# Optimization experiments

Measured on AMD Instinct MI355X. Metric: run time of the kernel, lower is better.

## Reference

```python
import jax, jax.numpy as jnp
import numpy as np

DIM = 256
N_CHANNELS = 8
NEIGHBORS = 16


def setup_inputs() -> dict:
    key = jax.random.key(0)
    kx, kw = jax.random.split(key)
    B, N, D = 4, 1024, DIM
    x = jax.random.normal(kx, (B, N, D), dtype=jnp.float32)
    # nn.Linear(dim, dim*2*n_channels, bias=False); store as [in, out] so y = x @ W
    W_qk = jax.random.normal(kw, (D, 2 * N_CHANNELS * D), dtype=jnp.float32) * (D ** -0.5)
    return {"x": x, "W_qk": W_qk}


def _norm_edge(edge):
    # edge: [B, C, N, N]
    norm_row = edge / (edge.sum(axis=-1, keepdims=True) + 1e-6)
    norm_col = norm_row / (norm_row.sum(axis=-2, keepdims=True) + 1e-6)
    # norm_row @ norm_col^T
    return jnp.einsum('bcnk,bcmk->bcnm', norm_row, norm_col)


def reference(x, W_qk):
    B, N, D = x.shape
    C = N_CHANNELS
    scale = D ** -0.5
    qk = (x @ W_qk).reshape(B, N, 2, C, D)
    q = jnp.transpose(qk[:, :, 0], (0, 2, 1, 3))  # [B, C, N, D]
    k = jnp.transpose(qk[:, :, 1], (0, 2, 1, 3))  # [B, C, N, D]
    attn = jax.nn.softmax(jnp.einsum('bcnd,bcmd->bcnm', q, k) * scale, axis=-1)

    # clip(): top-k neighbor mask from channel-summed (detached) attention
    sum_edge = jax.lax.stop_gradient(attn).sum(axis=1)  # [B, N, N]
    kk = min(NEIGHBORS, N)
    _, top_idx = jax.lax.top_k(sum_edge, kk)  # [B, N, kk]
    b_idx = jnp.arange(B)[:, None, None]
    r_idx = jnp.arange(N)[None, :, None]
    mask = jnp.zeros((B, N, N), dtype=attn.dtype).at[b_idx, r_idx, top_idx].set(1.0)
    mask = jnp.maximum(mask, jnp.eye(N, dtype=attn.dtype))  # identity diag
    edge = mask[:, None] * attn  # [B, C, N, N]
    return _norm_edge(edge)
```

## Files before the change

kernel.cpp:

```cpp
#include <hip/hip_runtime.h>
#include <hip/hip_bf16.h>
#include <math.h>

#define BB 4
#define NN 1024
#define DD 256
#define CC 8
#define KNBR 16
#define MAXSEL 17
#define ZCAP (NN * MAXSEL)

typedef _Float16 f16x8_t __attribute__((ext_vector_type(8)));
typedef _Float16 f16x4_t __attribute__((ext_vector_type(4)));
typedef float    f32x4_t __attribute__((ext_vector_type(4)));

__device__ __forceinline__ void gl2lds16(const _Float16* g, _Float16* ldsbase) {
    __builtin_amdgcn_global_load_lds(
        (const __attribute__((address_space(1))) unsigned int*)g,
        (__attribute__((address_space(3))) unsigned int*)ldsbase, 16, 0, 0);
}

__device__ __forceinline__ void split2(float v, _Float16& h, _Float16& l) {
    h = (_Float16)v;
    l = (_Float16)(v - (float)h);
}

__global__ __launch_bounds__(256) void split_all(const float* __restrict__ x,
                                                 const float* __restrict__ W,
                                                 _Float16* __restrict__ xh,
                                                 _Float16* __restrict__ xl,
                                                 _Float16* __restrict__ Wth,
                                                 _Float16* __restrict__ Wtl,
                                                 int* __restrict__ countb) {
    const int tid = threadIdx.x;
    if (blockIdx.x < 1024) {
        int i = (blockIdx.x * 256 + tid) * 4;
        float4 v = *(const float4*)(x + i);
        f16x4_t hv, lv;
        _Float16 h, l;
        split2(v.x, h, l); hv[0] = h; lv[0] = l;
        split2(v.y, h, l); hv[1] = h; lv[1] = l;
        split2(v.z, h, l); hv[2] = h; lv[2] = l;
        split2(v.w, h, l); hv[3] = h; lv[3] = l;
        *(f16x4_t*)(xh + i) = hv;
        *(f16x4_t*)(xl + i) = lv;
    } else {
        const int b2 = blockIdx.x - 1024;
        if (b2 == 0) {
            int4 zz = make_int4(0, 0, 0, 0);
#pragma unroll
            for (int g = 0; g < 4; g++) ((int4*)countb)[tid + 256 * g] = zz;
        }
        __shared__ float t[64][65];
        const int n0 = (b2 & 63) * 64;
        const int k0 = (b2 >> 6) * 64;
#pragma unroll
        for (int i = 0; i < 16; i++) {
            int k = i * 4 + (tid >> 6);
            int n = tid & 63;
            t[k][n] = W[(size_t)(k0 + k) * 4096 + n0 + n];
        }
        __syncthreads();
#pragma unroll
        for (int i = 0; i < 16; i++) {
            int n = i * 4 + (tid >> 6);
            int k = tid & 63;
            _Float16 h, l;
            split2(t[k][n] * 16.f, h, l);
            size_t o = (size_t)(n0 + n) * 256 + k0 + k;
            Wth[o] = h; Wtl[o] = l;
        }
    }
}

#define STG(dst, src, rowbase, kk)                                             \
    do {                                                                       \
        gl2lds16((src) + (size_t)((rowbase) + r_st) * 256 + (kk) + c8,         \
                 &(dst)[(w * 64) * 8]);                                        \
        gl2lds16((src) + (size_t)((rowbase) + 64 + r_st) * 256 + (kk) + c8,    \
                 &(dst)[(256 + w * 64) * 8]);                                  \
    } while (0)

#define MFMA3(accv, AH, AL, BH, BL)                                            \
    do {                                                                       \
        accv = __builtin_amdgcn_mfma_f32_16x16x32_f16(AL, BH, accv, 0, 0, 0);  \
        accv = __builtin_amdgcn_mfma_f32_16x16x32_f16(AH, BL, accv, 0, 0, 0);  \
        accv = __builtin_amdgcn_mfma_f32_16x16x32_f16(AH, BH, accv, 0, 0, 0);  \
    } while (0)

#define COMPUTE(AH, AL, BH, BL)                                                \
    do {                                                                       \
        f16x8_t ah[4], al[4];                                                  \
        _Pragma("unroll")                                                      \
        for (int mi = 0; mi < 4; mi++) {                                       \
            int r = (wr * 64 + mi * 16 + lm) * 32 + qx8;                       \
            ah[mi] = *(const f16x8_t*)&(AH)[r];                                \
            al[mi] = *(const f16x8_t*)&(AL)[r];                                \
        }                                                                      \
        _Pragma("unroll")                                                      \
        for (int ni = 0; ni < 4; ni++) {                                       \
            int rb = (wc * 64 + ni * 16 + lm) * 32 + qx8;                      \
            f16x8_t bh = *(const f16x8_t*)&(BH)[rb];                           \
            f16x8_t bl = *(const f16x8_t*)&(BL)[rb];                           \
            _Pragma("unroll")                                                  \
            for (int mi = 0; mi < 4; mi++)                                     \
                MFMA3(acc[mi][ni], ah[mi], al[mi], bh, bl);                    \
        }                                                                      \
    } while (0)

__global__ __launch_bounds__(256) void gemm_xw_mfma(
        const _Float16* __restrict__ xh, const _Float16* __restrict__ xl,
        const _Float16* __restrict__ wth, const _Float16* __restrict__ wtl,
        _Float16* __restrict__ qh, _Float16* __restrict__ ql,
        _Float16* __restrict__ kh, _Float16* __restrict__ kl) {
    __shared__ __align__(16) char smem[65536];
    _Float16* Ah0 = (_Float16*)smem;
    _Float16* Al0 = (_Float16*)(smem + 8192);
    _Float16* Bh0 = (_Float16*)(smem + 16384);
    _Float16* Bl0 = (_Float16*)(smem + 24576);
    _Float16* Ah1 = (_Float16*)(smem + 32768);
    _Float16* Al1 = (_Float16*)(smem + 40960);
    _Float16* Bh1 = (_Float16*)(smem + 49152);
    _Float16* Bl1 = (_Float16*)(smem + 57344);
    const int tid = threadIdx.x, lane = tid & 63, w = tid >> 6;
    const int wr = w >> 1, wc = w & 1;
    const int lm = lane & 15, quad = lane >> 4;
    const int row0 = blockIdx.y * 128, col0 = blockIdx.x * 128;
    const int r_st = tid >> 2;
    const int c8 = (((tid & 3) ^ ((tid >> 3) & 3)) * 8);
    const int qx8 = ((quad ^ ((lm >> 1) & 3)) * 8);

    f32x4_t acc[4][4];
#pragma unroll
    for (int i = 0; i < 4; i++)
#pragma unroll
        for (int j = 0; j < 4; j++) acc[i][j] = (f32x4_t)(0.f);

    STG(Ah0, xh, row0, 0); STG(Al0, xl, row0, 0);
    STG(Bh0, wth, col0, 0); STG(Bl0, wtl, col0, 0);
    __syncthreads();
#pragma unroll
    for (int t = 0; t < 8; t += 2) {
        {
            int kn = (t + 1) * 32;
            if (t + 1 < 8) {
                STG(Ah1, xh, row0, kn); STG(Al1, xl, row0, kn);
                STG(Bh1, wth, col0, kn); STG(Bl1, wtl, col0, kn);
            }
            COMPUTE(Ah0, Al0, Bh0, Bl0);
            __syncthreads();
        }
        {
            int kn = (t + 2) * 32;
            if (t + 2 < 8) {
                STG(Ah0, xh, row0, kn); STG(Al0, xl, row0, kn);
                STG(Bh0, wth, col0, kn); STG(Bl0, wtl, col0, kn);
            }
            COMPUTE(Ah1, Al1, Bh1, Bl1);
            __syncthreads();
        }
    }

    float* tr = (float*)smem;
    const int s = col0 >> 11, c = (col0 >> 8) & 7, dbase = col0 & 255;
    _Float16* dh = s ? kh : qh;
    _Float16* dl = s ? kl : ql;
    const int rl = tid >> 2;
    const int cb = (tid & 3) * 8;
#pragma unroll
    for (int p = 0; p < 2; p++) {
        if (p) __syncthreads();
        if (wr == p) {
#pragma unroll
            for (int mi = 0; mi < 4; mi++) {
                int rloc = mi * 16 + quad * 4;
#pragma unroll
                for (int ni = 0; ni < 4; ni++) {
                    int cl = wc * 64 + ni * 16 + lm;
#pragma unroll
                    for (int r = 0; r < 4; r++)
                        tr[(rloc + r) * 132 + cl] = acc[mi][ni][r];
                }
            }
        }
        __syncthreads();
        int rr = row0 + p * 64 + rl;
        int bb = rr >> 10, n = rr & 1023;
        size_t base = (((size_t)(bb * CC + c)) * NN + n) * DD + dbase;
#pragma unroll
        for (int g = 0; g < 4; g++) {
            int ccol = g * 32 + cb;
            f16x8_t hv, lv;
#pragma unroll
            for (int e = 0; e < 8; e++) {
                float vv = tr[rl * 132 + ccol + e];
                _Float16 h, l;
                split2(vv, h, l);
                hv[e] = h; lv[e] = l;
            }
            *(f16x8_t*)(dh + base + ccol) = hv;
            *(f16x8_t*)(dl + base + ccol) = lv;
        }
    }
}

__global__ __launch_bounds__(256) void gemm_qkt_mfma(
        const _Float16* __restrict__ qh, const _Float16* __restrict__ ql,
        const _Float16* __restrict__ kh, const _Float16* __restrict__ kl,
        float* __restrict__ attn) {
    __shared__ __align__(16) char smem[65536];
    _Float16* Ah0 = (_Float16*)smem;
    _Float16* Al0 = (_Float16*)(smem + 8192);
    _Float16* Bh0 = (_Float16*)(smem + 16384);
    _Float16* Bl0 = (_Float16*)(smem + 24576);
    _Float16* Ah1 = (_Float16*)(smem + 32768);
    _Float16* Al1 = (_Float16*)(smem + 40960);
    _Float16* Bh1 = (_Float16*)(smem + 49152);
    _Float16* Bl1 = (_Float16*)(smem + 57344);
    const int tid = threadIdx.x, lane = tid & 63, w = tid >> 6;
    const int wr = w >> 1, wc = w & 1;
    const int lm = lane & 15, quad = lane >> 4;
    const int id = blockIdx.x;
    const int rb8 = id & 7, qq = id >> 3;
    const int j = qq & 63, zhi = qq >> 6;
    const int z = zhi * 8 + rb8;
    const int row0 = (j >> 3) * 128, col0 = (j & 7) * 128;
    const size_t zo = (size_t)z * NN * DD;
    float* Cm = attn + (size_t)z * NN * NN;
    const int r_st = tid >> 2;
    const int c8 = (((tid & 3) ^ ((tid >> 3) & 3)) * 8);
    const int qx8 = ((quad ^ ((lm >> 1) & 3)) * 8);
    const float scale = 0.0625f / 256.0f;

    f32x4_t acc[4][4];
#pragma unroll
    for (int i = 0; i < 4; i++)
#pragma unroll
        for (int j2 = 0; j2 < 4; j2++) acc[i][j2] = (f32x4_t)(0.f);

    const _Float16* qhz = qh + zo;
    const _Float16* qlz = ql + zo;
    const _Float16* khz = kh + zo;
    const _Float16* klz = kl + zo;

    STG(Ah0, qhz, row0, 0); STG(Al0, qlz, row0, 0);
    STG(Bh0, khz, col0, 0); STG(Bl0, klz, col0, 0);
    __syncthreads();
#pragma unroll
    for (int t = 0; t < 8; t += 2) {
        {
            int kn = (t + 1) * 32;
            if (t + 1 < 8) {
                STG(Ah1, qhz, row0, kn); STG(Al1, qlz, row0, kn);
                STG(Bh1, khz, col0, kn); STG(Bl1, klz, col0, kn);
            }
            COMPUTE(Ah0, Al0, Bh0, Bl0);
            __syncthreads();
        }
        {
            int kn = (t + 2) * 32;
            if (t + 2 < 8) {
                STG(Ah0, qhz, row0, kn); STG(Al0, qlz, row0, kn);
                STG(Bh0, khz, col0, kn); STG(Bl0, klz, col0, kn);
            }
            COMPUTE(Ah1, Al1, Bh1, Bl1);
            __syncthreads();
        }
    }

#pragma unroll
    for (int mi = 0; mi < 4; mi++)
#pragma unroll
        for (int ni = 0; ni < 4; ni++) {
            int row = row0 + wr * 64 + mi * 16 + quad * 4;
            int col = col0 + wc * 64 + ni * 16 + lm;
#pragma unroll
            for (int r = 0; r < 4; r++)
                Cm[(size_t)(row + r) * NN + col] = acc[mi][ni][r] * scale;
        }
}

__global__ __launch_bounds__(256) void softmax_topk(const float* __restrict__ attn,
                                                    float2* __restrict__ ml,
                                                    int* __restrict__ idx,
                                                    int* __restrict__ cnt,
                                                    int* __restrict__ countb,
                                                    float* __restrict__ colsum) {
    __shared__ float sum[NN];
    __shared__ float wsc[CC][8];
    __shared__ float tv[4];
    __shared__ int ti[4];
    __shared__ int fsel[MAXSEL];
    __shared__ int fcnt;
    const int bn = blockIdx.x, b = bn >> 10, n = bn & 1023;
    const int tid = threadIdx.x, lane = tid & 63, w = tid >> 6;
    const int m4 = tid * 4;

    if (tid < CC) colsum[(size_t)(b * CC + tid) * NN + n] = 0.f;

    float4 s4 = make_float4(0.f, 0.f, 0.f, 0.f);
#pragma unroll
    for (int c = 0; c < CC; c++) {
        float4 v = *(const float4*)(attn + (((size_t)(b * CC + c) * NN + n) * NN + m4));
        float mx = fmaxf(fmaxf(v.x, v.y), fmaxf(v.z, v.w));
#pragma unroll
        for (int off = 32; off; off >>= 1) mx = fmaxf(mx, __shfl_down(mx, off));
        if (lane == 0) wsc[c][w] = mx;
        __syncthreads();
        mx = fmaxf(fmaxf(wsc[c][0], wsc[c][1]), fmaxf(wsc[c][2], wsc[c][3]));
        v.x = expf(v.x - mx); v.y = expf(v.y - mx);
        v.z = expf(v.z - mx); v.w = expf(v.w - mx);
        float sm = v.x + v.y + v.z + v.w;
#pragma unroll
        for (int off = 32; off; off >>= 1) sm += __shfl_down(sm, off);
        if (lane == 0) wsc[c][4 + w] = sm;
        __syncthreads();
        float l = wsc[c][4] + wsc[c][5] + wsc[c][6] + wsc[c][7];
        if (tid == 0) ml[(size_t)(b * CC + c) * NN + n] = make_float2(mx, l);
        float inv = 1.0f / l;
        s4.x += v.x * inv; s4.y += v.y * inv; s4.z += v.z * inv; s4.w += v.w * inv;
    }
    *(float4*)&sum[m4] = s4;
    __syncthreads();

    for (int it = 0; it < KNBR; it++) {
        float bv = sum[m4]; int bi = m4;
#pragma unroll
        for (int j = 1; j < 4; j++) {
            float x = sum[m4 + j];
            if (x > bv) { bv = x; bi = m4 + j; }
        }
#pragma unroll
        for (int off = 32; off; off >>= 1) {
            float ov = __shfl_down(bv, off);
            int oi = __shfl_down(bi, off);
            if (ov > bv || (ov == bv && oi < bi)) { bv = ov; bi = oi; }
        }
        if (lane == 0) { tv[w] = bv; ti[w] = bi; }
        __syncthreads();
        if (tid == 0) {
            float cv = tv[0]; int ci = ti[0];
#pragma unroll
            for (int k = 1; k < 4; k++)
                if (tv[k] > cv || (tv[k] == cv && ti[k] < ci)) { cv = tv[k]; ci = ti[k]; }
            fsel[it] = ci;
            sum[ci] = -INFINITY;
        }
        __syncthreads();
    }
    if (tid == 0) {
        bool has = false;
        for (int t = 0; t < KNBR; t++)
            if (fsel[t] == n) has = true;
        int c = KNBR;
        if (!has) { fsel[KNBR] = n; c = KNBR + 1; }
        fcnt = c;
        cnt[bn] = c;
    }
    __syncthreads();
    if (tid < fcnt) {
        idx[bn * MAXSEL + tid] = fsel[tid];
        atomicAdd(&countb[b * NN + fsel[tid]], 1);
    }
}

__global__ __launch_bounds__(256) void scan_offb(const int* __restrict__ countb,
                                                 int* __restrict__ offb,
                                                 int* __restrict__ curs) {
    __shared__ int wtot[4];
    const int b = blockIdx.x, tid = threadIdx.x, lane = tid & 63, w = tid >> 6;
    int c0 = countb[b * NN + tid * 4 + 0];
    int c1 = countb[b * NN + tid * 4 + 1];
    int c2 = countb[b * NN + tid * 4 + 2];
    int c3 = countb[b * NN + tid * 4 + 3];
    int tsum = c0 + c1 + c2 + c3;
    int incl = tsum;
#pragma unroll
    for (int off = 1; off < 64; off <<= 1) {
        int v = __shfl_up(incl, off);
        if (lane >= off) incl += v;
    }
    if (lane == 63) wtot[w] = incl;
    __syncthreads();
    int woff = 0;
    for (int i = 0; i < w; i++) woff += wtot[i];
    int base = woff + incl - tsum;
    int o0 = base, o1 = base + c0, o2 = base + c0 + c1, o3 = base + c0 + c1 + c2;
    offb[b * NN + tid * 4 + 0] = o0;
    offb[b * NN + tid * 4 + 1] = o1;
    offb[b * NN + tid * 4 + 2] = o2;
    offb[b * NN + tid * 4 + 3] = o3;
#pragma unroll
    for (int c = 0; c < CC; c++) {
        int z = b * CC + c;
        curs[z * NN + tid * 4 + 0] = o0;
        curs[z * NN + tid * 4 + 1] = o1;
        curs[z * NN + tid * 4 + 2] = o2;
        curs[z * NN + tid * 4 + 3] = o3;
    }
}

__global__ __launch_bounds__(256) void rownorm_fill(const float* __restrict__ attn,
                                                    const float2* __restrict__ ml,
                                                    const int* __restrict__ idx,
                                                    const int* __restrict__ cnt,
                                                    int* __restrict__ curs,
                                                    float* __restrict__ nr,
                                                    float* __restrict__ colsum,
                                                    int* __restrict__ eidx,
                                                    float* __restrict__ eval) {
    const int t = blockIdx.x * 256 + threadIdx.x;
    const int z = t >> 10, n = t & 1023;
    const int b = z >> 3;
    const int bn = b * NN + n;
    const int c_ = cnt[bn];
    const float* arow = attn + (size_t)t * NN;
    const float2 MM = ml[t];
    const float invl = 1.0f / MM.y;
    const size_t zb = (size_t)z * ZCAP;
    float a[MAXSEL];
    int kk[MAXSEL];
    float s = 0.f;
#pragma unroll
    for (int j = 0; j < MAXSEL; j++) {
        if (j < c_) {
            kk[j] = idx[bn * MAXSEL + j];
            float p = expf(arow[kk[j]] - MM.x) * invl;
            a[j] = p; s += p;
        }
    }
    const float inv = 1.f / (s + 1e-6f);
#pragma unroll
    for (int j = 0; j < MAXSEL; j++) {
        if (j < c_) {
            float v = a[j] * inv;
            nr[(size_t)t * MAXSEL + j] = v;
            atomicAdd(&colsum[(size_t)z * NN + kk[j]], v);
            int p = atomicAdd(&curs[z * NN + kk[j]], 1);
            eidx[zb + p] = n;
            eval[zb + p] = v;
        }
    }
}

__global__ __launch_bounds__(256) void out_sparse(const float* __restrict__ nr,
                                                  const int* __restrict__ idx,
                                                  const int* __restrict__ cnt,
                                                  const int* __restrict__ offb,
                                                  const int* __restrict__ countb,
                                                  const float* __restrict__ colsum,
                                                  const int* __restrict__ eidx,
                                                  const float* __restrict__ eval,
                                                  float* __restrict__ out) {
    __shared__ float row[NN];
    __shared__ float gscale[MAXSEL];
    __shared__ int goff[MAXSEL];
    __shared__ int glen[MAXSEL];
    const int t = blockIdx.x;
    const int z = t >> 10;
    const int b = z >> 3;
    const int bn = b * NN + (t & 1023);
    const int tid = threadIdx.x;
    const size_t zb = (size_t)z * ZCAP;

    ((float4*)row)[tid] = make_float4(0.f, 0.f, 0.f, 0.f);
    const int c_ = cnt[bn];
    if (tid < MAXSEL) {
        float sc = 0.f;
        int off = 0, len = 0;
        if (tid < c_) {
            int k = idx[bn * MAXSEL + tid];
            float wgt = nr[(size_t)t * MAXSEL + tid];
            sc = wgt / (colsum[(size_t)z * NN + k] + 1e-6f);
            off = offb[b * NN + k];
            len = countb[b * NN + k];
        }
        gscale[tid] = sc; goff[tid] = off; glen[tid] = len;
    }
    __syncthreads();
    const int j = tid / 15;
    const int lg = tid - j * 15;
    if (j < MAXSEL) {
        const float sc = gscale[j];
        const int off = goff[j], len = glen[j];
        for (int i = lg; i < len; i += 15) {
            int m = eidx[zb + off + i];
            float v = eval[zb + off + i];
            atomicAdd(&row[m], sc * v);
        }
    }
    __syncthreads();
    *(float4*)(out + (size_t)t * NN + tid * 4) = ((float4*)row)[tid];
}

extern "C" void kernel_launch(void* const* d_in, const int* in_sizes, int n_in,
                              void* d_out, int out_size, void* d_ws, size_t ws_size,
                              hipStream_t stream) {
    const float* x = (const float*)d_in[0];
    const float* W = (const float*)d_in[1];
    float* out = (float*)d_out;
    char* ws = (char*)d_ws;

    float* attn = (float*)d_out;

    _Float16* qh  = (_Float16*)(ws);
    _Float16* ql  = (_Float16*)(ws + 16777216ull);
    _Float16* kh  = (_Float16*)(ws + 33554432ull);
    _Float16* kl  = (_Float16*)(ws + 50331648ull);
    _Float16* xh  = (_Float16*)(ws + 67108864ull);
    _Float16* xl  = (_Float16*)(ws + 69206016ull);
    _Float16* wth = (_Float16*)(ws + 71303168ull);
    _Float16* wtl = (_Float16*)(ws + 73400320ull);
    int*    idx  = (int*)   (ws + 75497472ull);
    int*    cnt  = (int*)   (ws + 75776000ull);
    float*  nr   = (float*) (ws + 75792384ull);
    float*  colsum = (float*)(ws + 78020608ull);
    float2* ml   = (float2*)(ws + 78151680ull);
    int*    countb = (int*) (ws + 78413824ull);
    int*    offb = (int*)   (ws + 78430208ull);
    int*    curs = (int*)   (ws + 78446592ull);
    int*    eidx = (int*)   (ws + 78577664ull);
    float*  eval = (float*) (ws + 80805888ull);

    split_all<<<1280, 256, 0, stream>>>(x, W, xh, xl, wth, wtl, countb);
    gemm_xw_mfma<<<dim3(32, 32), 256, 0, stream>>>(xh, xl, wth, wtl,
                                                   qh, ql, kh, kl);
    gemm_qkt_mfma<<<2048, 256, 0, stream>>>(qh, ql, kh, kl, attn);
    softmax_topk<<<4096, 256, 0, stream>>>(attn, ml, idx, cnt, countb, colsum);
    scan_offb<<<4, 256, 0, stream>>>(countb, offb, curs);
    rownorm_fill<<<128, 256, 0, stream>>>(attn, ml, idx, cnt, curs, nr, colsum,
                                          eidx, eval);
    out_sparse<<<32768, 256, 0, stream>>>(nr, idx, cnt, offb, countb, colsum,
                                          eidx, eval, out);
}
```

Baseline: 411.8 us.

## Restructure softmax_topk with per-wave channel softmax and two-level warp top-k

Each wave now handles two full channel rows with wave-local max/sum reductions, so the per-channel block barriers are gone, and the partial channel sums are combined through shared memory. Top-k first runs independently inside each wave, which keeps 16 candidates per wave without block syncs, and wave 0 then merges the 64 candidates. This cuts the number of __syncthreads from about 50 to 3 per block, at the cost of more registers per thread (16-element buffers) and a larger shared-memory footprint.

```diff
diff --git a/kernel.cpp b/kernel.cpp
--- a/kernel.cpp
+++ b/kernel.cpp
@@ -286,76 +286,109 @@
                                                     int* __restrict__ cnt,
                                                     int* __restrict__ countb,
                                                     float* __restrict__ colsum) {
-    __shared__ float sum[NN];
-    __shared__ float wsc[CC][8];
-    __shared__ float tv[4];
-    __shared__ int ti[4];
+    __shared__ float psum[4][NN];
+    __shared__ float cval[64];
+    __shared__ int   cidx[64];
     __shared__ int fsel[MAXSEL];
     __shared__ int fcnt;
     const int bn = blockIdx.x, b = bn >> 10, n = bn & 1023;
     const int tid = threadIdx.x, lane = tid & 63, w = tid >> 6;
+
+    if (tid < CC) colsum[(size_t)(b * CC + tid) * NN + n] = 0.f;
+
+    const int colb = lane * 16;
+    float4 u[2][4];
+#pragma unroll
+    for (int p = 0; p < 2; p++) {
+        const int c = w * 2 + p;
+        const float* rowp = attn + (((size_t)(b * CC + c) * NN + n) * NN) + colb;
+#pragma unroll
+        for (int g = 0; g < 4; g++) u[p][g] = *(const float4*)(rowp + g * 4);
+    }
+
+    float acc[16];
+#pragma unroll
+    for (int e = 0; e < 16; e++) acc[e] = 0.f;
+
+#pragma unroll
+    for (int p = 0; p < 2; p++) {
+        const int c = w * 2 + p;
+        const float* f = (const float*)&u[p][0];
+        float mx = f[0];
+#pragma unroll
+        for (int e = 1; e < 16; e++) mx = fmaxf(mx, f[e]);
+#pragma unroll
+        for (int off = 1; off < 64; off <<= 1) mx = fmaxf(mx, __shfl_xor(mx, off));
+        float sm = 0.f;
+        float pe[16];
+#pragma unroll
+        for (int e = 0; e < 16; e++) { pe[e] = expf(f[e] - mx); sm += pe[e]; }
+#pragma unroll
+        for (int off = 1; off < 64; off <<= 1) sm += __shfl_xor(sm, off);
+        if (lane == 0) ml[(size_t)(b * CC + c) * NN + n] = make_float2(mx, sm);
+        float inv = 1.0f / sm;
+#pragma unroll
+        for (int e = 0; e < 16; e++) acc[e] += pe[e] * inv;
+    }
+#pragma unroll
+    for (int g = 0; g < 4; g++)
+        *(float4*)&psum[w][colb + g * 4] =
+            make_float4(acc[g * 4], acc[g * 4 + 1], acc[g * 4 + 2], acc[g * 4 + 3]);
+    __syncthreads();
+
     const int m4 = tid * 4;
-
-    if (tid < CC) colsum[(size_t)(b * CC + tid) * NN + n] = 0.f;
-
-    float4 s4 = make_float4(0.f, 0.f, 0.f, 0.f);
-#pragma unroll
-    for (int c = 0; c < CC; c++) {
-        float4 v = *(const float4*)(attn + (((size_t)(b * CC + c) * NN + n) * NN + m4));
-        float mx = fmaxf(fmaxf(v.x, v.y), fmaxf(v.z, v.w));
-#pragma unroll
-        for (int off = 32; off; off >>= 1) mx = fmaxf(mx, __shfl_down(mx, off));
-        if (lane == 0) wsc[c][w] = mx;
-        __syncthreads();
-        mx = fmaxf(fmaxf(wsc[c][0], wsc[c][1]), fmaxf(wsc[c][2], wsc[c][3]));
-        v.x = expf(v.x - mx); v.y = expf(v.y - mx);
-        v.z = expf(v.z - mx); v.w = expf(v.w - mx);
-        float sm = v.x + v.y + v.z + v.w;
-#pragma unroll
-        for (int off = 32; off; off >>= 1) sm += __shfl_down(sm, off);
-        if (lane == 0) wsc[c][4 + w] = sm;
-        __syncthreads();
-        float l = wsc[c][4] + wsc[c][5] + wsc[c][6] + wsc[c][7];
-        if (tid == 0) ml[(size_t)(b * CC + c) * NN + n] = make_float2(mx, l);
-        float inv = 1.0f / l;
-        s4.x += v.x * inv; s4.y += v.y * inv; s4.z += v.z * inv; s4.w += v.w * inv;
-    }
-    *(float4*)&sum[m4] = s4;
-    __syncthreads();
-
+    float4 a0 = *(const float4*)&psum[0][m4];
+    float4 a1 = *(const float4*)&psum[1][m4];
+    float4 a2 = *(const float4*)&psum[2][m4];
+    float4 a3 = *(const float4*)&psum[3][m4];
+    float v0 = a0.x + a1.x + a2.x + a3.x;
+    float v1 = a0.y + a1.y + a2.y + a3.y;
+    float v2 = a0.z + a1.z + a2.z + a3.z;
+    float v3 = a0.w + a1.w + a2.w + a3.w;
+
+    float myv = 0.f; int myi = 0;
     for (int it = 0; it < KNBR; it++) {
-        float bv = sum[m4]; int bi = m4;
-#pragma unroll
-        for (int j = 1; j < 4; j++) {
-            float x = sum[m4 + j];
-            if (x > bv) { bv = x; bi = m4 + j; }
-        }
-#pragma unroll
-        for (int off = 32; off; off >>= 1) {
-            float ov = __shfl_down(bv, off);
-            int oi = __shfl_down(bi, off);
+        float bv = v0; int bi = m4;
+        if (v1 > bv) { bv = v1; bi = m4 + 1; }
+        if (v2 > bv) { bv = v2; bi = m4 + 2; }
+        if (v3 > bv) { bv = v3; bi = m4 + 3; }
+#pragma unroll
+        for (int off = 1; off < 64; off <<= 1) {
+            float ov = __shfl_xor(bv, off);
+            int oi = __shfl_xor(bi, off);
             if (ov > bv || (ov == bv && oi < bi)) { bv = ov; bi = oi; }
         }
-        if (lane == 0) { tv[w] = bv; ti[w] = bi; }
-        __syncthreads();
-        if (tid == 0) {
-            float cv = tv[0]; int ci = ti[0];
-#pragma unroll
-            for (int k = 1; k < 4; k++)
-                if (tv[k] > cv || (tv[k] == cv && ti[k] < ci)) { cv = tv[k]; ci = ti[k]; }
-            fsel[it] = ci;
-            sum[ci] = -INFINITY;
-        }
-        __syncthreads();
-    }
-    if (tid == 0) {
-        bool has = false;
-        for (int t = 0; t < KNBR; t++)
-            if (fsel[t] == n) has = true;
-        int c = KNBR;
-        if (!has) { fsel[KNBR] = n; c = KNBR + 1; }
-        fcnt = c;
-        cnt[bn] = c;
+        if (lane == it) { myv = bv; myi = bi; }
+        v0 = (bi == m4)     ? -INFINITY : v0;
+        v1 = (bi == m4 + 1) ? -INFINITY : v1;
+        v2 = (bi == m4 + 2) ? -INFINITY : v2;
+        v3 = (bi == m4 + 3) ? -INFINITY : v3;
+    }
+    if (lane < KNBR) { cval[w * KNBR + lane] = myv; cidx[w * KNBR + lane] = myi; }
+    __syncthreads();
+
+    if (w == 0) {
+        float mv = cval[lane]; int mi = cidx[lane];
+        for (int it = 0; it < KNBR; it++) {
+            float bv = mv; int bi = mi;
+#pragma unroll
+            for (int off = 1; off < 64; off <<= 1) {
+                float ov = __shfl_xor(bv, off);
+                int oi = __shfl_xor(bi, off);
+                if (ov > bv || (ov == bv && oi < bi)) { bv = ov; bi = oi; }
+            }
+            if (lane == 0) fsel[it] = bi;
+            if (mi == bi) mv = -INFINITY;
+        }
+        if (lane == 0) {
+            bool has = false;
+            for (int t = 0; t < KNBR; t++)
+                if (fsel[t] == n) has = true;
+            int c = KNBR;
+            if (!has) { fsel[KNBR] = n; c = KNBR + 1; }
+            fcnt = c;
+            cnt[bn] = c;
+        }
     }
     __syncthreads();
     if (tid < fcnt) {
```

Measured after the change: 411.8 us. No clear change (+0.0%).
